# Performance work log

Measured on AMD Instinct MI355X. Metric: run time of the kernel, lower is better.

The kernel has to match this reference:

```python
import jax, jax.numpy as jnp
import numpy as np
import math

D_MODEL, N_HEADS, D_FF = 512, 8, 2048
B, S = 4, 2048
EPS = 1e-6


def _layernorm(x, alpha, bias):
    # Faithful to the torch module: std is unbiased (ddof=1) and eps is added to std, not var.
    m = jnp.mean(x, axis=-1, keepdims=True)
    s = jnp.std(x, axis=-1, keepdims=True, ddof=1)
    return alpha * (x - m) / (s + EPS) + bias


def setup_inputs() -> dict:
    key = jax.random.key(0)
    ks = jax.random.split(key, 16)
    d, f = D_MODEL, D_FF
    sd = 1.0 / math.sqrt(d)
    sf = 1.0 / math.sqrt(f)
    return {
        "x": jax.random.normal(ks[0], (B, S, d), jnp.float32),
        "wq": jax.random.normal(ks[1], (d, d), jnp.float32) * sd,
        "bq": jnp.zeros((d,), jnp.float32),
        "wk": jax.random.normal(ks[2], (d, d), jnp.float32) * sd,
        "bk": jnp.zeros((d,), jnp.float32),
        "wv": jax.random.normal(ks[3], (d, d), jnp.float32) * sd,
        "bv": jnp.zeros((d,), jnp.float32),
        "wo": jax.random.normal(ks[4], (d, d), jnp.float32) * sd,
        "bo": jnp.zeros((d,), jnp.float32),
        "w1": jax.random.normal(ks[5], (d, f), jnp.float32) * sd,
        "b1": jnp.zeros((f,), jnp.float32),
        "w2": jax.random.normal(ks[6], (f, d), jnp.float32) * sf,
        "b2": jnp.zeros((d,), jnp.float32),
        "ln1_a": jnp.ones((d,), jnp.float32),
        "ln1_b": jnp.zeros((d,), jnp.float32),
        "ln2_a": jnp.ones((d,), jnp.float32),
        "ln2_b": jnp.zeros((d,), jnp.float32),
    }


def reference(x, wq, bq, wk, bk, wv, bv, wo, bo, w1, b1, w2, b2, ln1_a, ln1_b, ln2_a, ln2_b):
    b, s, d = x.shape
    h, dk = N_HEADS, d // N_HEADS
    # QKV projections -> [b, h, s, dk]
    q = (x @ wq + bq).reshape(b, s, h, dk).transpose(0, 2, 1, 3)
    k = (x @ wk + bk).reshape(b, s, h, dk).transpose(0, 2, 1, 3)
    v = (x @ wv + bv).reshape(b, s, h, dk).transpose(0, 2, 1, 3)
    # Manual scaled-dot-product attention (no mask in EncoderBlock path)
    scores = jnp.einsum("bhqd,bhkd->bhqk", q, k) / jnp.sqrt(jnp.float32(dk))
    probs = jax.nn.softmax(scores, axis=-1)
    attn = jnp.einsum("bhqk,bhkd->bhqd", probs, v)
    concat = attn.transpose(0, 2, 1, 3).reshape(b, s, d)
    mha_out = concat @ wo + bo
    # Residual + LayerNorm 1
    y = _layernorm(x + mha_out, ln1_a, ln1_b)
    # FFN + Residual + LayerNorm 2
    ff = jax.nn.relu(y @ w1 + b1) @ w2 + b2
    return _layernorm(y + ff, ln2_a, ln2_b)
```

## Files before the change

kernel.cpp:

```cpp
#include <hip/hip_runtime.h>
#include <hip/hip_bf16.h>


typedef __bf16 bf16;
typedef __bf16 bf16x4 __attribute__((ext_vector_type(4)));
typedef __bf16 bf16x8 __attribute__((ext_vector_type(8)));
typedef float  f32x4  __attribute__((ext_vector_type(4)));

#define NBATCH 4
#define SEQ    2048
#define DMODEL 512
#define NHEADS 8
#define DHEAD  64
#define DFF    2048
#define MTOT   (NBATCH * SEQ)
#define WS_NEED 73416712u

__device__ __forceinline__ f32x4 mfma16(bf16x8 a, bf16x8 b, f32x4 c) {
    return __builtin_amdgcn_mfma_f32_16x16x32_bf16(a, b, c, 0, 0, 0);
}

__device__ __forceinline__ void lds16(const bf16* g, bf16* l) {
    __builtin_amdgcn_global_load_lds(
        (const __attribute__((address_space(1))) void*)g,
        (__attribute__((address_space(3))) void*)l, 16, 0, 0);
}

__device__ __forceinline__ float load_in(const void* src, size_t i, int mode) {
    float f = mode ? ((const float*)src)[i] : (float)((const bf16*)src)[i];
    if (!(fabsf(f) < 1e30f)) f = 0.f;
    return f;
}

__global__ void sentinel_kernel(bf16* out) {
    out[threadIdx.x] = (bf16)1000.0f;
}

__global__ __launch_bounds__(256) void detect_mode(const unsigned int* x_raw,
                                                   int* flag) {
    __shared__ int cnt[256];
    int t = threadIdx.x, c = 0;
#pragma unroll
    for (int j = 0; j < 4; j++) {
        unsigned int w = x_raw[t * 4 + j];
        unsigned int e = (w >> 7) & 0xFF;
        c += (e >= 100 && e <= 135) ? 1 : 0;
    }
    cnt[t] = c;
    __syncthreads();
    for (int s = 128; s > 0; s >>= 1) {
        if (t < s) cnt[t] += cnt[t + s];
        __syncthreads();
    }
    if (t == 0) *flag = (cnt[0] >= 512) ? 0 : 1;
}

__global__ __launch_bounds__(256) void convert_to_bf16_v4(
        const void* __restrict__ src, bf16* __restrict__ dst, int n,
        const int* __restrict__ modep) {
    int mode = *modep;
    int i = (blockIdx.x * 256 + threadIdx.x) * 4;
    if (i >= n) return;
    float f0, f1, f2, f3;
    if (mode) {
        float4 f = *(const float4*)((const float*)src + i);
        f0 = f.x; f1 = f.y; f2 = f.z; f3 = f.w;
    } else {
        bf16x4 v = *(const bf16x4*)((const bf16*)src + i);
        f0 = (float)v[0]; f1 = (float)v[1]; f2 = (float)v[2]; f3 = (float)v[3];
    }
    if (!(fabsf(f0) < 1e30f)) f0 = 0.f;
    if (!(fabsf(f1) < 1e30f)) f1 = 0.f;
    if (!(fabsf(f2) < 1e30f)) f2 = 0.f;
    if (!(fabsf(f3) < 1e30f)) f3 = 0.f;
    bf16x4 o = {(bf16)f0, (bf16)f1, (bf16)f2, (bf16)f3};
    *(bf16x4*)(dst + i) = o;
}

__global__ __launch_bounds__(256) void convert_params(
        const void* s0, const void* s1, const void* s2, const void* s3,
        const void* s4, const void* s5, const void* s6, const void* s7,
        const void* s8, const void* s9,
        bf16* __restrict__ prm, const int* __restrict__ modep) {
    const void* srcs[10] = {s0, s1, s2, s3, s4, s5, s6, s7, s8, s9};
    const int   len[10]  = {512, 512, 512, 512, 2048, 512, 512, 512, 512, 512};
    const int   dst[10]  = {0, 512, 1024, 1536, 2048, 4096, 4608, 5120, 5632, 6144};
    int b = blockIdx.x;
    int mode = *modep;
    const void* s = srcs[b];
    bf16* d = prm + dst[b];
    for (int i = threadIdx.x; i < len[b]; i += 256)
        d[i] = (bf16)load_in(s, i, mode);
}

__global__ __launch_bounds__(256) void transpose4_512(
        const void* s0, const void* s1, const void* s2, const void* s3,
        bf16* __restrict__ out, const int* __restrict__ modep) {
    __shared__ bf16 tile[32][33];
    const void* srcs[4] = {s0, s1, s2, s3};
    const void* in = srcs[blockIdx.z];
    bf16* o = out + (size_t)blockIdx.z * 262144;
    int mode = *modep;
    int n0 = blockIdx.x * 32, k0 = blockIdx.y * 32;
    int tx = threadIdx.x, ty = threadIdx.y;
#pragma unroll
    for (int i = 0; i < 4; i++) {
        int kl = ty * 4 + i;
        tile[kl][tx] = (bf16)load_in(in, (size_t)(k0 + kl) * 512 + n0 + tx, mode);
    }
    __syncthreads();
#pragma unroll
    for (int i = 0; i < 4; i++) {
        int nl = ty * 4 + i;
        o[(size_t)(n0 + nl) * 512 + k0 + tx] = tile[tx][nl];
    }
}

__global__ __launch_bounds__(256) void transpose_bf16(
        const void* __restrict__ in, bf16* __restrict__ out, int K, int N,
        const int* __restrict__ modep) {
    __shared__ bf16 tile[32][33];
    int mode = *modep;
    int n0 = blockIdx.x * 32, k0 = blockIdx.y * 32;
    int tx = threadIdx.x, ty = threadIdx.y;
#pragma unroll
    for (int i = 0; i < 4; i++) {
        int kl = ty * 4 + i;
        tile[kl][tx] = (bf16)load_in(in, (size_t)(k0 + kl) * N + n0 + tx, mode);
    }
    __syncthreads();
#pragma unroll
    for (int i = 0; i < 4; i++) {
        int nl = ty * 4 + i;
        out[(size_t)(n0 + nl) * K + k0 + tx] = tile[tx][nl];
    }
}

template <bool RELU>
__global__ __launch_bounds__(256) void gemm_bt(
        const bf16* __restrict__ A, const bf16* __restrict__ BT,
        const bf16* __restrict__ bias, bf16* __restrict__ Cout,
        int M, int N, int K) {
    constexpr int BM = 128, BN = 128, BK = 32;
    __shared__ __align__(16) bf16 As[BM * BK];
    __shared__ __align__(16) bf16 Bs[BN * BK];

    int tid  = threadIdx.x;
    int wid  = tid >> 6, lane = tid & 63;
    int quad = lane >> 4, l15 = lane & 15;
    int mb = blockIdx.x * BM, nb = blockIdx.y * BN;
    int wm = (wid >> 1) * 64, wn = (wid & 1) * 64;

    f32x4 acc[4][4] = {};

    int c0 = wid * 128 + lane;
    int c1 = c0 + 64;
    int ar0 = c0 >> 2, ac0 = (c0 & 3) * 8;
    int ar1 = c1 >> 2, ac1 = (c1 & 3) * 8;
    bf16* lA0 = &As[(wid * 2 + 0) * 512];
    bf16* lA1 = &As[(wid * 2 + 1) * 512];
    bf16* lB0 = &Bs[(wid * 2 + 0) * 512];
    bf16* lB1 = &Bs[(wid * 2 + 1) * 512];

    for (int k0 = 0; k0 < K; k0 += BK) {
        __syncthreads();
        lds16(&A [(size_t)(mb + ar0) * K + k0 + ac0], lA0);
        lds16(&A [(size_t)(mb + ar1) * K + k0 + ac1], lA1);
        lds16(&BT[(size_t)(nb + ar0) * K + k0 + ac0], lB0);
        lds16(&BT[(size_t)(nb + ar1) * K + k0 + ac1], lB1);
        __syncthreads();

        bf16x8 af[4], bfr[4];
#pragma unroll
        for (int i = 0; i < 4; i++)
            af[i] = *(const bf16x8*)&As[(wm + i * 16 + l15) * 32 + quad * 8];
#pragma unroll
        for (int j = 0; j < 4; j++)
            bfr[j] = *(const bf16x8*)&Bs[(wn + j * 16 + l15) * 32 + quad * 8];
#pragma unroll
        for (int i = 0; i < 4; i++)
#pragma unroll
            for (int j = 0; j < 4; j++)
                acc[i][j] = mfma16(af[i], bfr[j], acc[i][j]);
    }

#pragma unroll
    for (int j = 0; j < 4; j++) {
        int n = nb + wn + j * 16 + l15;
        float bv = (float)bias[n];
#pragma unroll
        for (int i = 0; i < 4; i++) {
            int mBase = mb + wm + i * 16 + quad * 4;
#pragma unroll
            for (int r = 0; r < 4; r++) {
                float v = acc[i][j][r] + bv;
                if (RELU) v = v > 0.f ? v : 0.f;
                Cout[(size_t)(mBase + r) * N + n] = (bf16)v;
            }
        }
    }
}

__global__ __launch_bounds__(256) void gemm_qkv(
        const bf16* __restrict__ A, const bf16* __restrict__ BT,
        const bf16* __restrict__ bias,
        bf16* __restrict__ Cq, bf16* __restrict__ Ck, bf16* __restrict__ Cv,
        int M, int N, int K) {
    constexpr int BM = 128, BN = 128, BK = 32;
    __shared__ __align__(16) bf16 As[BM * BK];
    __shared__ __align__(16) bf16 Bs[BN * BK];

    int tid  = threadIdx.x;
    int wid  = tid >> 6, lane = tid & 63;
    int quad = lane >> 4, l15 = lane & 15;
    int mb = blockIdx.x * BM, nb = blockIdx.y * BN;
    int wm = (wid >> 1) * 64, wn = (wid & 1) * 64;

    f32x4 acc[4][4] = {};

    int c0 = wid * 128 + lane;
    int c1 = c0 + 64;
    int ar0 = c0 >> 2, ac0 = (c0 & 3) * 8;
    int ar1 = c1 >> 2, ac1 = (c1 & 3) * 8;
    bf16* lA0 = &As[(wid * 2 + 0) * 512];
    bf16* lA1 = &As[(wid * 2 + 1) * 512];
    bf16* lB0 = &Bs[(wid * 2 + 0) * 512];
    bf16* lB1 = &Bs[(wid * 2 + 1) * 512];

    for (int k0 = 0; k0 < K; k0 += BK) {
        __syncthreads();
        lds16(&A [(size_t)(mb + ar0) * K + k0 + ac0], lA0);
        lds16(&A [(size_t)(mb + ar1) * K + k0 + ac1], lA1);
        lds16(&BT[(size_t)(nb + ar0) * K + k0 + ac0], lB0);
        lds16(&BT[(size_t)(nb + ar1) * K + k0 + ac1], lB1);
        __syncthreads();

        bf16x8 af[4], bfr[4];
#pragma unroll
        for (int i = 0; i < 4; i++)
            af[i] = *(const bf16x8*)&As[(wm + i * 16 + l15) * 32 + quad * 8];
#pragma unroll
        for (int j = 0; j < 4; j++)
            bfr[j] = *(const bf16x8*)&Bs[(wn + j * 16 + l15) * 32 + quad * 8];
#pragma unroll
        for (int i = 0; i < 4; i++)
#pragma unroll
            for (int j = 0; j < 4; j++)
                acc[i][j] = mfma16(af[i], bfr[j], acc[i][j]);
    }

    int reg = nb >> 9;
    bf16* C = (reg == 0) ? Cq : (reg == 1) ? Ck : Cv;
#pragma unroll
    for (int j = 0; j < 4; j++) {
        int n = nb + wn + j * 16 + l15;
        float bv = (float)bias[n];
        int nn = n & 511;
        int h = nn >> 6, dk = nn & 63;
#pragma unroll
        for (int i = 0; i < 4; i++) {
            int mBase = mb + wm + i * 16 + quad * 4;
#pragma unroll
            for (int r = 0; r < 4; r++) {
                float v = acc[i][j][r] + bv;
                int m = mBase + r;
                int b = m >> 11, s = m & (SEQ - 1);
                if (reg < 2)
                    C[((size_t)(b * NHEADS + h) * SEQ + s) * DHEAD + dk] = (bf16)v;
                else
                    C[((size_t)(b * NHEADS + h) * DHEAD + dk) * SEQ + s] = (bf16)v;
            }
        }
    }
}

__global__ __launch_bounds__(256) void attn_kernel(
        const bf16* __restrict__ Q, const bf16* __restrict__ K,
        const bf16* __restrict__ VT, bf16* __restrict__ Out) {
    __shared__ __align__(16) bf16 Ks[2][64 * 72];
    __shared__ __align__(16) bf16 Vs[2][64 * 72];
    __shared__ __align__(16) bf16 Pb[4][2][16 * 72];
    int tid  = threadIdx.x;
    int wid  = tid >> 6, lane = tid & 63;
    int quad = lane >> 4, l15 = lane & 15;
    int bh = blockIdx.y;
    int qb = blockIdx.x * 128 + wid * 32;

    const bf16* Qh = Q  + (size_t)bh * SEQ * DHEAD;
    const bf16* Kh = K  + (size_t)bh * SEQ * DHEAD;
    const bf16* Vh = VT + (size_t)bh * DHEAD * SEQ;

    bf16x8 bQ0[2], bQ1[2];
#pragma unroll
    for (int c = 0; c < 2; c++) {
        const bf16* qp = &Qh[(qb + c * 16 + l15) * DHEAD + quad * 8];
        bQ0[c] = *(const bf16x8*)qp;
        bQ1[c] = *(const bf16x8*)(qp + 32);
    }

    int cc0 = tid * 2, cc1 = cc0 + 1;
    int kr0 = cc0 >> 3, kc0 = (cc0 & 7) * 8;
    int kr1 = cc1 >> 3, kc1 = (cc1 & 7) * 8;

    float lrow[2] = {0.f, 0.f};
    f32x4 Oacc[2][4] = {};

    {
        uint4 ka0 = *(const uint4*)&Kh[(size_t)kr0 * DHEAD + kc0];
        uint4 ka1 = *(const uint4*)&Kh[(size_t)kr1 * DHEAD + kc1];
        uint4 va0 = *(const uint4*)&Vh[(size_t)kr0 * SEQ + kc0];
        uint4 va1 = *(const uint4*)&Vh[(size_t)kr1 * SEQ + kc1];
        *(uint4*)&Ks[0][kr0 * 72 + kc0] = ka0;
        *(uint4*)&Ks[0][kr1 * 72 + kc1] = ka1;
        *(uint4*)&Vs[0][kr0 * 72 + kc0] = va0;
        *(uint4*)&Vs[0][kr1 * 72 + kc1] = va1;
    }
    __syncthreads();

    for (int it = 0; it < SEQ / 64; it++) {
        int cur = it & 1, nxt = cur ^ 1;
        int kb = (it + 1) * 64;
        uint4 nk0, nk1, nv0, nv1;
        bool pf = (it + 1 < SEQ / 64);
        if (pf) {
            nk0 = *(const uint4*)&Kh[(size_t)(kb + kr0) * DHEAD + kc0];
            nk1 = *(const uint4*)&Kh[(size_t)(kb + kr1) * DHEAD + kc1];
            nv0 = *(const uint4*)&Vh[(size_t)kr0 * SEQ + kb + kc0];
            nv1 = *(const uint4*)&Vh[(size_t)kr1 * SEQ + kb + kc1];
        }

        bf16x8 aK0[4], aK1[4], bV0[4], bV1[4];
#pragma unroll
        for (int t = 0; t < 4; t++) {
            const bf16* kp = &Ks[cur][(t * 16 + l15) * 72 + quad * 8];
            aK0[t] = *(const bf16x8*)kp;
            aK1[t] = *(const bf16x8*)(kp + 32);
            const bf16* vp = &Vs[cur][(t * 16 + l15) * 72 + quad * 8];
            bV0[t] = *(const bf16x8*)vp;
            bV1[t] = *(const bf16x8*)(vp + 32);
        }

#pragma unroll
        for (int c = 0; c < 2; c++) {
            f32x4 st[4];
#pragma unroll
            for (int t = 0; t < 4; t++) {
                f32x4 z = {0.f, 0.f, 0.f, 0.f};
                st[t] = mfma16(aK1[t], bQ1[c], mfma16(aK0[t], bQ0[c], z));
            }
            bf16* myP = Pb[wid][c];
#pragma unroll
            for (int t = 0; t < 4; t++) {
                bf16x4 pk;
                float ps = 0.f;
#pragma unroll
                for (int r = 0; r < 4; r++) {
                    float s = fminf(fmaxf(st[t][r] * 0.125f, -60.f), 60.f);
                    float p = __expf(s);
                    ps += p;
                    pk[r] = (bf16)p;
                }
                lrow[c] += ps;
                *(bf16x4*)&myP[l15 * 72 + t * 16 + quad * 4] = pk;
            }
            bf16x8 aP0 = *(const bf16x8*)&myP[l15 * 72 + quad * 8];
            bf16x8 aP1 = *(const bf16x8*)&myP[l15 * 72 + 32 + quad * 8];
#pragma unroll
            for (int nt = 0; nt < 4; nt++)
                Oacc[c][nt] = mfma16(aP1, bV1[nt],
                                     mfma16(aP0, bV0[nt], Oacc[c][nt]));
        }

        if (pf) {
            *(uint4*)&Ks[nxt][kr0 * 72 + kc0] = nk0;
            *(uint4*)&Ks[nxt][kr1 * 72 + kc1] = nk1;
            *(uint4*)&Vs[nxt][kr0 * 72 + kc0] = nv0;
            *(uint4*)&Vs[nxt][kr1 * 72 + kc1] = nv1;
        }
        __syncthreads();
    }

    int b = bh >> 3, hd = bh & 7;
#pragma unroll
    for (int c = 0; c < 2; c++) {
        float l = lrow[c];
        l += __shfl_xor(l, 16);
        l += __shfl_xor(l, 32);
        float linv[4];
#pragma unroll
        for (int r = 0; r < 4; r++)
            linv[r] = 1.f / __shfl(l, quad * 4 + r);
#pragma unroll
        for (int nt = 0; nt < 4; nt++)
#pragma unroll
            for (int r = 0; r < 4; r++) {
                int s = qb + c * 16 + quad * 4 + r;
                Out[((size_t)(b * SEQ + s)) * DMODEL + hd * 64 + nt * 16 + l15]
                    = (bf16)(Oacc[c][nt][r] * linv[r]);
            }
    }
}

__global__ __launch_bounds__(256) void ln_kernel(
        const bf16* __restrict__ X, const bf16* __restrict__ T,
        const bf16* __restrict__ Al, const bf16* __restrict__ Bl,
        void* __restrict__ Out, const int* __restrict__ modep, int final_out) {
    int mode = *modep;
    int wid = threadIdx.x >> 6, lane = threadIdx.x & 63;
    int row = blockIdx.x * 4 + wid;
    const bf16* xr = X + (size_t)row * DMODEL;
    const bf16* tr = T + (size_t)row * DMODEL;
    bf16x8 xv = *(const bf16x8*)&xr[lane * 8];
    bf16x8 tv = *(const bf16x8*)&tr[lane * 8];
    float v[8];
#pragma unroll
    for (int i = 0; i < 8; i++) v[i] = (float)xv[i] + (float)tv[i];
    float sum = 0.f, sq = 0.f;
#pragma unroll
    for (int i = 0; i < 8; i++) { sum += v[i]; sq += v[i] * v[i]; }
#pragma unroll
    for (int m = 1; m < 64; m <<= 1) {
        sum += __shfl_xor(sum, m);
        sq  += __shfl_xor(sq,  m);
    }
    float mean = sum * (1.f / DMODEL);
    float var  = (sq - DMODEL * mean * mean) * (1.f / (DMODEL - 1));
    var = var > 0.f ? var : 0.f;
    float inv = 1.f / (sqrtf(var) + 1e-6f);
#pragma unroll
    for (int i = 0; i < 8; i++) {
        int c = lane * 8 + i;
        float yv = (float)Al[c] * (v[i] - mean) * inv + (float)Bl[c];
        yv = fminf(fmaxf(yv, -1e4f), 1e4f);
        size_t idx = (size_t)row * DMODEL + c;
        if (final_out && mode) ((float*)Out)[idx] = yv;
        else                   ((bf16*)Out)[idx]  = (bf16)yv;
    }
}

extern "C" void kernel_launch(void* const* d_in, const int* in_sizes, int n_in,
                              void* d_out, int out_size, void* d_ws, size_t ws_size,
                              hipStream_t stream) {
    if (ws_size < WS_NEED) {
        sentinel_kernel<<<1, 64, 0, stream>>>((bf16*)d_out);
        return;
    }

    const void* x  = d_in[0];
    const void* wq = d_in[1],  *bq = d_in[2];
    const void* wk = d_in[3],  *bk = d_in[4];
    const void* wv = d_in[5],  *bv = d_in[6];
    const void* wo = d_in[7],  *bo = d_in[8];
    const void* w1 = d_in[9],  *b1 = d_in[10];
    const void* w2 = d_in[11], *b2 = d_in[12];
    const void* ln1a = d_in[13], *ln1b = d_in[14];
    const void* ln2a = d_in[15], *ln2b = d_in[16];

    char* ws = (char*)d_ws;
    bf16* wqT  = (bf16*)(ws + 0);
    bf16* woT  = (bf16*)(ws + 1572864);
    bf16* w1T  = (bf16*)(ws + 2097152);
    bf16* w2T  = (bf16*)(ws + 4194304);
    bf16* xcv  = (bf16*)(ws + 6291456);
    bf16* prm  = (bf16*)(ws + 14680064);
    bf16* regA = (bf16*)(ws + 14696448);
    bf16* regB = (bf16*)(ws + 23085056);
    bf16* regC = (bf16*)(ws + 31473664);
    bf16* ff1  = (bf16*)(ws + 39862272);
    int*  modep = (int*)(ws + 73416704);
    bf16* aout = (bf16*)d_out;

    bf16 *pbq = prm, *pbo = prm + 1536;
    bf16 *pb1 = prm + 2048, *pb2 = prm + 4096;
    bf16 *pl1a = prm + 4608, *pl1b = prm + 5120;
    bf16 *pl2a = prm + 5632, *pl2b = prm + 6144;

    detect_mode<<<1, 256, 0, stream>>>((const unsigned int*)x, modep);

    convert_to_bf16_v4<<<4096, 256, 0, stream>>>(x, xcv, MTOT * DMODEL, modep);
    convert_params<<<10, 256, 0, stream>>>(bq, bk, bv, bo, b1, b2,
                                           ln1a, ln1b, ln2a, ln2b, prm, modep);

    dim3 tb(32, 8);
    transpose4_512<<<dim3(16, 16, 4), tb, 0, stream>>>(wq, wk, wv, wo, wqT, modep);
    transpose_bf16<<<dim3(64, 16), tb, 0, stream>>>(w1, w1T, DMODEL, DFF, modep);
    transpose_bf16<<<dim3(16, 64), tb, 0, stream>>>(w2, w2T, DFF, DMODEL, modep);

    gemm_qkv<<<dim3(64, 12), 256, 0, stream>>>(xcv, wqT, pbq,
                                               regA, regB, regC,
                                               MTOT, 3 * DMODEL, DMODEL);

    attn_kernel<<<dim3(SEQ / 128, NBATCH * NHEADS), 256, 0, stream>>>(
        regA, regB, regC, aout);

    gemm_bt<false><<<dim3(64, 4), 256, 0, stream>>>(aout, woT, pbo, regA, MTOT, DMODEL, DMODEL);

    ln_kernel<<<MTOT / 4, 256, 0, stream>>>(xcv, regA, pl1a, pl1b, regB, modep, 0);

    gemm_bt<true ><<<dim3(64, 16), 256, 0, stream>>>(regB, w1T, pb1, ff1, MTOT, DFF, DMODEL);
    gemm_bt<false><<<dim3(64, 4),  256, 0, stream>>>(ff1, w2T, pb2, regA, MTOT, DMODEL, DFF);

    ln_kernel<<<MTOT / 4, 256, 0, stream>>>(regB, regA, pl2a, pl2b, d_out, modep, 1);
}
```

Measured before the change: 322.5 us.

## Drop dtype detection, merge prep kernels, fold Q scale, stage V transpose, add BM64 GEMM

Removes the runtime input-dtype detection and assumes fp32 inputs. The weight transposes and parameter conversions are merged into a single prep launch. The 1/sqrt(dk) scale is folded into the Q projection epilogue, and the V transpose store goes through LDS so it can be written as coalesced 16-byte chunks. Adds a 64-row-tile GEMM for the N=512 output projections to double the block count. This cuts launch count and scattered stores, but bf16 inputs are no longer supported and the extra LDS buffer in gemm_qkv may reduce occupancy.

```diff
diff --git a/kernel.cpp b/kernel.cpp
--- a/kernel.cpp
+++ b/kernel.cpp
@@ -26,107 +26,62 @@
         (__attribute__((address_space(3))) void*)l, 16, 0, 0);
 }
 
-__device__ __forceinline__ float load_in(const void* src, size_t i, int mode) {
-    float f = mode ? ((const float*)src)[i] : (float)((const bf16*)src)[i];
-    if (!(fabsf(f) < 1e30f)) f = 0.f;
-    return f;
+__device__ __forceinline__ float scrub(float f) {
+    return (fabsf(f) < 1e30f) ? f : 0.f;
 }
 
 __global__ void sentinel_kernel(bf16* out) {
     out[threadIdx.x] = (bf16)1000.0f;
 }
 
-__global__ __launch_bounds__(256) void detect_mode(const unsigned int* x_raw,
-                                                   int* flag) {
-    __shared__ int cnt[256];
-    int t = threadIdx.x, c = 0;
-#pragma unroll
-    for (int j = 0; j < 4; j++) {
-        unsigned int w = x_raw[t * 4 + j];
-        unsigned int e = (w >> 7) & 0xFF;
-        c += (e >= 100 && e <= 135) ? 1 : 0;
-    }
-    cnt[t] = c;
-    __syncthreads();
-    for (int s = 128; s > 0; s >>= 1) {
-        if (t < s) cnt[t] += cnt[t + s];
-        __syncthreads();
-    }
-    if (t == 0) *flag = (cnt[0] >= 512) ? 0 : 1;
-}
-
-__global__ __launch_bounds__(256) void convert_to_bf16_v4(
-        const void* __restrict__ src, bf16* __restrict__ dst, int n,
-        const int* __restrict__ modep) {
-    int mode = *modep;
+__global__ __launch_bounds__(256) void convert_x(
+        const float* __restrict__ src, bf16* __restrict__ dst) {
     int i = (blockIdx.x * 256 + threadIdx.x) * 4;
-    if (i >= n) return;
-    float f0, f1, f2, f3;
-    if (mode) {
-        float4 f = *(const float4*)((const float*)src + i);
-        f0 = f.x; f1 = f.y; f2 = f.z; f3 = f.w;
+    float4 f = *(const float4*)(src + i);
+    bf16x4 o = {(bf16)scrub(f.x), (bf16)scrub(f.y),
+                (bf16)scrub(f.z), (bf16)scrub(f.w)};
+    *(bf16x4*)(dst + i) = o;
+}
+
+__global__ __launch_bounds__(256) void prep_kernel(
+        const float* wq, const float* wk, const float* wv, const float* wo,
+        const float* w1, const float* w2,
+        const float* bq, const float* bk, const float* bv, const float* bo,
+        const float* b1, const float* b2,
+        const float* l1a, const float* l1b, const float* l2a, const float* l2b,
+        bf16* __restrict__ wT, bf16* __restrict__ w1T, bf16* __restrict__ w2T,
+        bf16* __restrict__ prm) {
+    __shared__ bf16 tile[32][33];
+    int b = blockIdx.x;
+    if (b < 10) {
+        const float* srcs[10] = {bq, bk, bv, bo, b1, b2, l1a, l1b, l2a, l2b};
+        const int len[10] = {512,512,512,512,2048,512,512,512,512,512};
+        const int dst[10] = {0,512,1024,1536,2048,4096,4608,5120,5632,6144};
+        const float* s = srcs[b];
+        bf16* d = prm + dst[b];
+        for (int i = threadIdx.x; i < len[b]; i += 256)
+            d[i] = (bf16)scrub(s[i]);
+        return;
+    }
+    const float* in; bf16* out; int K, N, bx, by;
+    if (b < 1034) {
+        int idx = b - 10, z = idx >> 8, rem = idx & 255;
+        const float* srcs[4] = {wq, wk, wv, wo};
+        in = srcs[z]; out = wT + (size_t)z * 262144;
+        K = 512; N = 512; bx = rem & 15; by = rem >> 4;
+    } else if (b < 2058) {
+        int idx = b - 1034;
+        in = w1; out = w1T; K = 512; N = 2048; bx = idx & 63; by = idx >> 6;
     } else {
-        bf16x4 v = *(const bf16x4*)((const bf16*)src + i);
-        f0 = (float)v[0]; f1 = (float)v[1]; f2 = (float)v[2]; f3 = (float)v[3];
-    }
-    if (!(fabsf(f0) < 1e30f)) f0 = 0.f;
-    if (!(fabsf(f1) < 1e30f)) f1 = 0.f;
-    if (!(fabsf(f2) < 1e30f)) f2 = 0.f;
-    if (!(fabsf(f3) < 1e30f)) f3 = 0.f;
-    bf16x4 o = {(bf16)f0, (bf16)f1, (bf16)f2, (bf16)f3};
-    *(bf16x4*)(dst + i) = o;
-}
-
-__global__ __launch_bounds__(256) void convert_params(
-        const void* s0, const void* s1, const void* s2, const void* s3,
-        const void* s4, const void* s5, const void* s6, const void* s7,
-        const void* s8, const void* s9,
-        bf16* __restrict__ prm, const int* __restrict__ modep) {
-    const void* srcs[10] = {s0, s1, s2, s3, s4, s5, s6, s7, s8, s9};
-    const int   len[10]  = {512, 512, 512, 512, 2048, 512, 512, 512, 512, 512};
-    const int   dst[10]  = {0, 512, 1024, 1536, 2048, 4096, 4608, 5120, 5632, 6144};
-    int b = blockIdx.x;
-    int mode = *modep;
-    const void* s = srcs[b];
-    bf16* d = prm + dst[b];
-    for (int i = threadIdx.x; i < len[b]; i += 256)
-        d[i] = (bf16)load_in(s, i, mode);
-}
-
-__global__ __launch_bounds__(256) void transpose4_512(
-        const void* s0, const void* s1, const void* s2, const void* s3,
-        bf16* __restrict__ out, const int* __restrict__ modep) {
-    __shared__ bf16 tile[32][33];
-    const void* srcs[4] = {s0, s1, s2, s3};
-    const void* in = srcs[blockIdx.z];
-    bf16* o = out + (size_t)blockIdx.z * 262144;
-    int mode = *modep;
-    int n0 = blockIdx.x * 32, k0 = blockIdx.y * 32;
-    int tx = threadIdx.x, ty = threadIdx.y;
+        int idx = b - 2058;
+        in = w2; out = w2T; K = 2048; N = 512; bx = idx & 15; by = idx >> 4;
+    }
+    int tx = threadIdx.x & 31, ty = threadIdx.x >> 5;
+    int n0 = bx * 32, k0 = by * 32;
 #pragma unroll
     for (int i = 0; i < 4; i++) {
         int kl = ty * 4 + i;
-        tile[kl][tx] = (bf16)load_in(in, (size_t)(k0 + kl) * 512 + n0 + tx, mode);
-    }
-    __syncthreads();
-#pragma unroll
-    for (int i = 0; i < 4; i++) {
-        int nl = ty * 4 + i;
-        o[(size_t)(n0 + nl) * 512 + k0 + tx] = tile[tx][nl];
-    }
-}
-
-__global__ __launch_bounds__(256) void transpose_bf16(
-        const void* __restrict__ in, bf16* __restrict__ out, int K, int N,
-        const int* __restrict__ modep) {
-    __shared__ bf16 tile[32][33];
-    int mode = *modep;
-    int n0 = blockIdx.x * 32, k0 = blockIdx.y * 32;
-    int tx = threadIdx.x, ty = threadIdx.y;
-#pragma unroll
-    for (int i = 0; i < 4; i++) {
-        int kl = ty * 4 + i;
-        tile[kl][tx] = (bf16)load_in(in, (size_t)(k0 + kl) * N + n0 + tx, mode);
+        tile[kl][tx] = (bf16)scrub(in[(size_t)(k0 + kl) * N + n0 + tx]);
     }
     __syncthreads();
 #pragma unroll
@@ -153,8 +108,7 @@
 
     f32x4 acc[4][4] = {};
 
-    int c0 = wid * 128 + lane;
-    int c1 = c0 + 64;
+    int c0 = wid * 128 + lane, c1 = c0 + 64;
     int ar0 = c0 >> 2, ac0 = (c0 & 3) * 8;
     int ar1 = c1 >> 2, ac1 = (c1 & 3) * 8;
     bf16* lA0 = &As[(wid * 2 + 0) * 512];
@@ -190,6 +144,70 @@
         float bv = (float)bias[n];
 #pragma unroll
         for (int i = 0; i < 4; i++) {
+            int mBase = mb + wm + i * 16 + quad * 4;
+#pragma unroll
+            for (int r = 0; r < 4; r++) {
+                float v = acc[i][j][r] + bv;
+                if (RELU) v = v > 0.f ? v : 0.f;
+                Cout[(size_t)(mBase + r) * N + n] = (bf16)v;
+            }
+        }
+    }
+}
+
+template <bool RELU>
+__global__ __launch_bounds__(256) void gemm_bt64(
+        const bf16* __restrict__ A, const bf16* __restrict__ BT,
+        const bf16* __restrict__ bias, bf16* __restrict__ Cout,
+        int M, int N, int K) {
+    constexpr int BM = 64, BN = 128, BK = 32;
+    __shared__ __align__(16) bf16 As[BM * BK];
+    __shared__ __align__(16) bf16 Bs[BN * BK];
+
+    int tid  = threadIdx.x;
+    int wid  = tid >> 6, lane = tid & 63;
+    int quad = lane >> 4, l15 = lane & 15;
+    int mb = blockIdx.x * BM, nb = blockIdx.y * BN;
+    int wm = (wid >> 1) * 32, wn = (wid & 1) * 64;
+
+    f32x4 acc[2][4] = {};
+
+    int cA = wid * 64 + lane;
+    int arA = cA >> 2, acA = (cA & 3) * 8;
+    int cB0 = wid * 128 + lane, cB1 = cB0 + 64;
+    int br0 = cB0 >> 2, bc0 = (cB0 & 3) * 8;
+    int br1 = cB1 >> 2, bc1 = (cB1 & 3) * 8;
+    bf16* lA  = &As[wid * 512];
+    bf16* lB0 = &Bs[(wid * 2 + 0) * 512];
+    bf16* lB1 = &Bs[(wid * 2 + 1) * 512];
+
+    for (int k0 = 0; k0 < K; k0 += BK) {
+        __syncthreads();
+        lds16(&A [(size_t)(mb + arA) * K + k0 + acA], lA);
+        lds16(&BT[(size_t)(nb + br0) * K + k0 + bc0], lB0);
+        lds16(&BT[(size_t)(nb + br1) * K + k0 + bc1], lB1);
+        __syncthreads();
+
+        bf16x8 af[2], bfr[4];
+#pragma unroll
+        for (int i = 0; i < 2; i++)
+            af[i] = *(const bf16x8*)&As[(wm + i * 16 + l15) * 32 + quad * 8];
+#pragma unroll
+        for (int j = 0; j < 4; j++)
+            bfr[j] = *(const bf16x8*)&Bs[(wn + j * 16 + l15) * 32 + quad * 8];
+#pragma unroll
+        for (int i = 0; i < 2; i++)
+#pragma unroll
+            for (int j = 0; j < 4; j++)
+                acc[i][j] = mfma16(af[i], bfr[j], acc[i][j]);
+    }
+
+#pragma unroll
+    for (int j = 0; j < 4; j++) {
+        int n = nb + wn + j * 16 + l15;
+        float bv = (float)bias[n];
+#pragma unroll
+        for (int i = 0; i < 2; i++) {
             int mBase = mb + wm + i * 16 + quad * 4;
 #pragma unroll
             for (int r = 0; r < 4; r++) {
@@ -209,6 +227,7 @@
     constexpr int BM = 128, BN = 128, BK = 32;
     __shared__ __align__(16) bf16 As[BM * BK];
     __shared__ __align__(16) bf16 Bs[BN * BK];
+    __shared__ __align__(16) bf16 Ts[128 * 136];
 
     int tid  = threadIdx.x;
     int wid  = tid >> 6, lane = tid & 63;
@@ -218,8 +237,7 @@
 
     f32x4 acc[4][4] = {};
 
-    int c0 = wid * 128 + lane;
-    int c1 = c0 + 64;
+    int c0 = wid * 128 + lane, c1 = c0 + 64;
     int ar0 = c0 >> 2, ac0 = (c0 & 3) * 8;
     int ar1 = c1 >> 2, ac1 = (c1 & 3) * 8;
     bf16* lA0 = &As[(wid * 2 + 0) * 512];
@@ -250,27 +268,51 @@
     }
 
     int reg = nb >> 9;
-    bf16* C = (reg == 0) ? Cq : (reg == 1) ? Ck : Cv;
-#pragma unroll
-    for (int j = 0; j < 4; j++) {
-        int n = nb + wn + j * 16 + l15;
-        float bv = (float)bias[n];
-        int nn = n & 511;
+    if (reg < 2) {
+        bf16* C = reg ? Ck : Cq;
+        float scl = reg ? 1.0f : 0.125f;
+#pragma unroll
+        for (int j = 0; j < 4; j++) {
+            int n = nb + wn + j * 16 + l15;
+            float bv = (float)bias[n];
+            int nn = n & 511;
+            int h = nn >> 6, dk = nn & 63;
+#pragma unroll
+            for (int i = 0; i < 4; i++) {
+                int mBase = mb + wm + i * 16 + quad * 4;
+#pragma unroll
+                for (int r = 0; r < 4; r++) {
+                    float v = (acc[i][j][r] + bv) * scl;
+                    int m = mBase + r;
+                    int b = m >> 11, s = m & (SEQ - 1);
+                    C[((size_t)(b * NHEADS + h) * SEQ + s) * DHEAD + dk] = (bf16)v;
+                }
+            }
+        }
+    } else {
+#pragma unroll
+        for (int j = 0; j < 4; j++) {
+            int nl = wn + j * 16 + l15;
+            float bv = (float)bias[nb + nl];
+#pragma unroll
+            for (int i = 0; i < 4; i++) {
+                int ml = wm + i * 16 + quad * 4;
+                bf16x4 pk;
+#pragma unroll
+                for (int r = 0; r < 4; r++) pk[r] = (bf16)(acc[i][j][r] + bv);
+                *(bf16x4*)&Ts[nl * 136 + ml] = pk;
+            }
+        }
+        __syncthreads();
+        int nl = tid >> 1, half = tid & 1;
+        int nn = (nb + nl) & 511;
         int h = nn >> 6, dk = nn & 63;
-#pragma unroll
-        for (int i = 0; i < 4; i++) {
-            int mBase = mb + wm + i * 16 + quad * 4;
-#pragma unroll
-            for (int r = 0; r < 4; r++) {
-                float v = acc[i][j][r] + bv;
-                int m = mBase + r;
-                int b = m >> 11, s = m & (SEQ - 1);
-                if (reg < 2)
-                    C[((size_t)(b * NHEADS + h) * SEQ + s) * DHEAD + dk] = (bf16)v;
-                else
-                    C[((size_t)(b * NHEADS + h) * DHEAD + dk) * SEQ + s] = (bf16)v;
-            }
-        }
+        int bb = mb >> 11, s0 = mb & (SEQ - 1);
+        bf16* dst = &Cv[((size_t)(bb * NHEADS + h) * DHEAD + dk) * SEQ + s0 + half * 64];
+        const bf16* srcl = &Ts[nl * 136 + half * 64];
+#pragma unroll
+        for (int v = 0; v < 8; v++)
+            *(uint4*)(dst + v * 8) = *(const uint4*)(srcl + v * 8);
     }
 }
 
@@ -355,8 +397,7 @@
                 float ps = 0.f;
 #pragma unroll
                 for (int r = 0; r < 4; r++) {
-                    float s = fminf(fmaxf(st[t][r] * 0.125f, -60.f), 60.f);
-                    float p = __expf(s);
+                    float p = __expf(fminf(st[t][r], 60.f));
                     ps += p;
                     pk[r] = (bf16)p;
                 }
@@ -404,8 +445,7 @@
 __global__ __launch_bounds__(256) void ln_kernel(
         const bf16* __restrict__ X, const bf16* __restrict__ T,
         const bf16* __restrict__ Al, const bf16* __restrict__ Bl,
-        void* __restrict__ Out, const int* __restrict__ modep, int final_out) {
-    int mode = *modep;
+        void* __restrict__ Out, int final_out) {
     int wid = threadIdx.x >> 6, lane = threadIdx.x & 63;
     int row = blockIdx.x * 4 + wid;
     const bf16* xr = X + (size_t)row * DMODEL;
@@ -433,8 +473,8 @@
         float yv = (float)Al[c] * (v[i] - mean) * inv + (float)Bl[c];
         yv = fminf(fmaxf(yv, -1e4f), 1e4f);
         size_t idx = (size_t)row * DMODEL + c;
-        if (final_out && mode) ((float*)Out)[idx] = yv;
-        else                   ((bf16*)Out)[idx]  = (bf16)yv;
+        if (final_out) ((float*)Out)[idx] = yv;
+        else           ((bf16*)Out)[idx]  = (bf16)yv;
     }
 }
 
@@ -446,18 +486,18 @@
         return;
     }
 
-    const void* x  = d_in[0];
-    const void* wq = d_in[1],  *bq = d_in[2];
-    const void* wk = d_in[3],  *bk = d_in[4];
-    const void* wv = d_in[5],  *bv = d_in[6];
-    const void* wo = d_in[7],  *bo = d_in[8];
-    const void* w1 = d_in[9],  *b1 = d_in[10];
-    const void* w2 = d_in[11], *b2 = d_in[12];
-    const void* ln1a = d_in[13], *ln1b = d_in[14];
-    const void* ln2a = d_in[15], *ln2b = d_in[16];
+    const float* x  = (const float*)d_in[0];
+    const float* wq = (const float*)d_in[1],  *bq = (const float*)d_in[2];
+    const float* wk = (const float*)d_in[3],  *bk = (const float*)d_in[4];
+    const float* wv = (const float*)d_in[5],  *bv = (const float*)d_in[6];
+    const float* wo = (const float*)d_in[7],  *bo = (const float*)d_in[8];
+    const float* w1 = (const float*)d_in[9],  *b1 = (const float*)d_in[10];
+    const float* w2 = (const float*)d_in[11], *b2 = (const float*)d_in[12];
+    const float* ln1a = (const float*)d_in[13], *ln1b = (const float*)d_in[14];
+    const float* ln2a = (const float*)d_in[15], *ln2b = (const float*)d_in[16];
 
     char* ws = (char*)d_ws;
-    bf16* wqT  = (bf16*)(ws + 0);
+    bf16* wT   = (bf16*)(ws + 0);
     bf16* woT  = (bf16*)(ws + 1572864);
     bf16* w1T  = (bf16*)(ws + 2097152);
     bf16* w2T  = (bf16*)(ws + 4194304);
@@ -467,7 +507,6 @@
     bf16* regB = (bf16*)(ws + 23085056);
     bf16* regC = (bf16*)(ws + 31473664);
     bf16* ff1  = (bf16*)(ws + 39862272);
-    int*  modep = (int*)(ws + 73416704);
     bf16* aout = (bf16*)d_out;
 
     bf16 *pbq = prm, *pbo = prm + 1536;
@@ -475,30 +514,28 @@
     bf16 *pl1a = prm + 4608, *pl1b = prm + 5120;
     bf16 *pl2a = prm + 5632, *pl2b = prm + 6144;
 
-    detect_mode<<<1, 256, 0, stream>>>((const unsigned int*)x, modep);
-
-    convert_to_bf16_v4<<<4096, 256, 0, stream>>>(x, xcv, MTOT * DMODEL, modep);
-    convert_params<<<10, 256, 0, stream>>>(bq, bk, bv, bo, b1, b2,
-                                           ln1a, ln1b, ln2a, ln2b, prm, modep);
-
-    dim3 tb(32, 8);
-    transpose4_512<<<dim3(16, 16, 4), tb, 0, stream>>>(wq, wk, wv, wo, wqT, modep);
-    transpose_bf16<<<dim3(64, 16), tb, 0, stream>>>(w1, w1T, DMODEL, DFF, modep);
-    transpose_bf16<<<dim3(16, 64), tb, 0, stream>>>(w2, w2T, DFF, DMODEL, modep);
-
-    gemm_qkv<<<dim3(64, 12), 256, 0, stream>>>(xcv, wqT, pbq,
+    convert_x<<<4096, 256, 0, stream>>>(x, xcv);
+    prep_kernel<<<3082, 256, 0, stream>>>(wq, wk, wv, wo, w1, w2,
+                                          bq, bk, bv, bo, b1, b2,
+                                          ln1a, ln1b, ln2a, ln2b,
+                                          wT, w1T, w2T, prm);
+
+    gemm_qkv<<<dim3(64, 12), 256, 0, stream>>>(xcv, wT, pbq,
                                                regA, regB, regC,
                                                MTOT, 3 * DMODEL, DMODEL);
 
     attn_kernel<<<dim3(SEQ / 128, NBATCH * NHEADS), 256, 0, stream>>>(
         regA, regB, regC, aout);
 
-    gemm_bt<false><<<dim3(64, 4), 256, 0, stream>>>(aout, woT, pbo, regA, MTOT, DMODEL, DMODEL);
-
-    ln_kernel<<<MTOT / 4, 256, 0, stream>>>(xcv, regA, pl1a, pl1b, regB, modep, 0);
-
-    gemm_bt<true ><<<dim3(64, 16), 256, 0, stream>>>(regB, w1T, pb1, ff1, MTOT, DFF, DMODEL);
-    gemm_bt<false><<<dim3(64, 4),  256, 0, stream>>>(ff1, w2T, pb2, regA, MTOT, DMODEL, DFF);
-
-    ln_kernel<<<MTOT / 4, 256, 0, stream>>>(regB, regA, pl2a, pl2b, d_out, modep, 1);
-}
+    gemm_bt64<false><<<dim3(128, 4), 256, 0, stream>>>(aout, woT, pbo, regA,
+                                                       MTOT, DMODEL, DMODEL);
+
+    ln_kernel<<<MTOT / 4, 256, 0, stream>>>(xcv, regA, pl1a, pl1b, regB, 0);
+
+    gemm_bt<true ><<<dim3(64, 16), 256, 0, stream>>>(regB, w1T, pb1, ff1,
+                                                     MTOT, DFF, DMODEL);
+    gemm_bt64<false><<<dim3(128, 4), 256, 0, stream>>>(ff1, w2T, pb2, regA,
+                                                       MTOT, DMODEL, DFF);
+
+    ln_kernel<<<MTOT / 4, 256, 0, stream>>>(regB, regA, pl2a, pl2b, d_out, 1);
+}
```

Result: faster. 293.0 us (-9.2%).
